# Kernel optimization log

Measured on AMD Instinct MI355X. Metric: run time of the kernel, lower is better.

The kernel has to match this reference:

```python
import jax, jax.numpy as jnp
import numpy as np

B, N, HID, HEADS, LAYERS, POOL = 2, 2048, 256, 4, 2, 128
D = HID // HEADS  # per-head dim


def attn_pool(x, w1, b1, w2, b2):
    # x: [B,N,HID]; mask is all-ones in this module's forward, so plain softmax
    s = jnp.tanh(x @ w1 + b1) @ w2 + b2            # [B,N]
    a = jax.nn.softmax(s, axis=-1)                  # [B,N]
    return jnp.einsum('bn,bnc->bc', a, x)           # [B,HID]


def gat_layer(x, adj_mask, proj_w, a_src, a_dst):
    # x: [B,N,HID] -> h: [B,N,HEADS,D]
    h = (x @ proj_w).reshape(x.shape[0], x.shape[1], HEADS, D)
    src = jnp.einsum('bnhd,hd->bnh', h, a_src)      # [B,N,H]
    dst = jnp.einsum('bnhd,hd->bnh', h, a_dst)      # [B,N,H]
    logits = src[:, :, None, :] + dst[:, None, :, :]  # [B,i,j,H]
    logits = jnp.where(logits >= 0, logits, 0.2 * logits)  # leaky_relu(0.2)
    logits = jnp.where(adj_mask[..., None], logits, jnp.float32(-1e9))
    attn = jax.nn.softmax(logits, axis=2)           # softmax over j (neighbors)
    out = jnp.einsum('bijh,bjhd->bihd', attn, h)
    return out.reshape(x.shape[0], x.shape[1], HEADS * D)


def setup_inputs() -> dict:
    key = jax.random.key(0)
    ks = jax.random.split(key, 16)
    sd = 0.05
    gene_expr = jax.random.normal(ks[0], (B, N), dtype=jnp.float32)
    gene_adj = jax.random.randint(ks[1], (B, N, N), 0, 2, dtype=jnp.int32)
    in_w = jax.random.normal(ks[2], (HID,), dtype=jnp.float32) * sd
    in_b = jax.random.normal(ks[3], (HID,), dtype=jnp.float32) * sd
    proj_w = jax.random.normal(ks[4], (LAYERS, HID, HID), dtype=jnp.float32) * sd
    attn_src = jax.random.normal(ks[5], (LAYERS, HEADS, D), dtype=jnp.float32) * sd
    attn_dst = jax.random.normal(ks[6], (LAYERS, HEADS, D), dtype=jnp.float32) * sd
    pool_w1 = jax.random.normal(ks[7], (LAYERS, HID, POOL), dtype=jnp.float32) * sd
    pool_b1 = jax.random.normal(ks[8], (LAYERS, POOL), dtype=jnp.float32) * sd
    pool_w2 = jax.random.normal(ks[9], (LAYERS, POOL), dtype=jnp.float32) * sd
    pool_b2 = jax.random.normal(ks[10], (LAYERS,), dtype=jnp.float32) * sd
    ip_w1 = jax.random.normal(ks[11], (HID, POOL), dtype=jnp.float32) * sd
    ip_b1 = jax.random.normal(ks[12], (POOL,), dtype=jnp.float32) * sd
    ip_w2 = jax.random.normal(ks[13], (POOL,), dtype=jnp.float32) * sd
    ip_b2 = jax.random.normal(ks[14], (), dtype=jnp.float32) * sd
    return dict(gene_expr=gene_expr, gene_adj=gene_adj, in_w=in_w, in_b=in_b,
                proj_w=proj_w, attn_src=attn_src, attn_dst=attn_dst,
                pool_w1=pool_w1, pool_b1=pool_b1, pool_w2=pool_w2, pool_b2=pool_b2,
                ip_w1=ip_w1, ip_b1=ip_b1, ip_w2=ip_w2, ip_b2=ip_b2)


def reference(gene_expr, gene_adj, in_w, in_b, proj_w, attn_src, attn_dst,
              pool_w1, pool_b1, pool_w2, pool_b2, ip_w1, ip_b1, ip_w2, ip_b2):
    # input_proj: Linear(1, HID) on gene_expr[...,None], then relu
    x = jax.nn.relu(gene_expr[:, :, None] * in_w + in_b)  # [B,N,HID]
    raw_pooled = attn_pool(x, ip_w1, ip_b1, ip_w2, ip_b2)
    adj_mask = gene_adj > 0
    node_outs, pooled_outs = [], []
    cur = x
    for l in range(LAYERS):
        cur = gat_layer(cur, adj_mask, proj_w[l], attn_src[l], attn_dst[l])
        cur = jax.nn.elu(cur)
        node_outs.append(cur)
        pooled_outs.append(attn_pool(cur, pool_w1[l], pool_b1[l], pool_w2[l], pool_b2[l]))
    # (raw_pooled, node_out_0, node_out_1, pooled_0, pooled_1); final_pooled == pooled_outs[-1]
    return (raw_pooled, *node_outs, *pooled_outs)
```

## Files before the change

kernel.cpp:

```cpp
#include <hip/hip_runtime.h>
#include <hip/hip_bf16.h>

#define B_ 2
#define N_ 2048
#define HID_ 256
#define HEADS_ 4
#define D_ 64
#define POOL_ 128
#define LOG2E_ 1.4426950408889634f

typedef __bf16 bf16;
typedef __bf16 bf16x8 __attribute__((ext_vector_type(8)));
typedef float f32x4 __attribute__((ext_vector_type(4)));

__device__ __forceinline__ float fast_tanh(float x) {
    x = fminf(fmaxf(x, -15.f), 15.f);
    float t = __expf(2.f * x);
    return (t - 1.f) / (t + 1.f);
}

__global__ void k_setup(const int* __restrict__ adj, unsigned* __restrict__ am,
                        const float* __restrict__ ge, const float* __restrict__ iw,
                        const float* __restrict__ ib, bf16* __restrict__ xb,
                        const float* __restrict__ proj_w, const float* __restrict__ ipw1,
                        const float* __restrict__ pw1, bf16* __restrict__ wT0,
                        bf16* __restrict__ wT1, bf16* __restrict__ ipw1T,
                        bf16* __restrict__ w1T0, bf16* __restrict__ w1T1) {
    int blk = blockIdx.x, tid = threadIdx.x;
    if (blk < 32768) {
        int gid = blk * 256 + tid;
        int v = adj[gid];
        unsigned long long mask = __ballot(v > 0);
        int lane = tid & 63;
        if (lane == 0) am[gid >> 5] = (unsigned)mask;
        else if (lane == 32) am[gid >> 5] = (unsigned)(mask >> 32);
    } else if (blk < 36864) {
        int row = blk - 32768;
        float g = ge[row];
        float v = fmaxf(g * iw[tid] + ib[tid], 0.f);
        xb[row * HID_ + tid] = (bf16)v;
    } else {
        int o = (blk - 36864) * 256 + tid;
        const float* src; bf16* dst; int Nc, loc;
        if (o < 65536)       { src = proj_w;         dst = wT0;   Nc = 256; loc = o; }
        else if (o < 131072) { src = proj_w + 65536; dst = wT1;   Nc = 256; loc = o - 65536; }
        else if (o < 163840) { src = ipw1;           dst = ipw1T; Nc = 128; loc = o - 131072; }
        else if (o < 196608) { src = pw1;            dst = w1T0;  Nc = 128; loc = o - 163840; }
        else                 { src = pw1 + 32768;    dst = w1T1;  Nc = 128; loc = o - 196608; }
        int n = loc >> 8, k = loc & 255;
        dst[loc] = (bf16)src[k * Nc + n];
    }
}

__device__ __forceinline__ void pool_sw_body(const bf16* __restrict__ A,
                                             const bf16* __restrict__ W1T,
                                             const float* __restrict__ b1,
                                             const float* __restrict__ w2,
                                             const float* __restrict__ b2,
                                             float* __restrict__ part,
                                             float* __restrict__ pz,
                                             int slot, int b, int ch, char* smemraw) {
    int n0 = ch * 16;
    int tid = threadIdx.x;
    int w = tid >> 6, lane = tid & 63, r = lane & 15, g = lane >> 4;
    const bf16* ap = A + ((long long)(b * N_ + n0) + r) * 256 + g * 8;
    f32x4 acc[2] = {{0,0,0,0},{0,0,0,0}};
    for (int ks = 0; ks < 256; ks += 32) {
        bf16x8 af = *(const bf16x8*)(ap + ks);
        #pragma unroll
        for (int nf = 0; nf < 2; ++nf) {
            bf16x8 bfr = *(const bf16x8*)(W1T + (w * 32 + nf * 16 + r) * 256 + ks + g * 8);
            acc[nf] = __builtin_amdgcn_mfma_f32_16x16x32_bf16(af, bfr, acc[nf], 0, 0, 0);
        }
    }
    float b1v[2], w2v[2];
    #pragma unroll
    for (int nf = 0; nf < 2; ++nf) {
        b1v[nf] = b1[w * 32 + nf * 16 + r];
        w2v[nf] = w2[w * 32 + nf * 16 + r];
    }
    float (*pred)[16] = (float (*)[16])smemraw;
    float* el = (float*)(smemraw + 256);
    #pragma unroll
    for (int q = 0; q < 4; ++q) {
        float p = fast_tanh(acc[0][q] + b1v[0]) * w2v[0] + fast_tanh(acc[1][q] + b1v[1]) * w2v[1];
        p += __shfl_xor(p, 1); p += __shfl_xor(p, 2);
        p += __shfl_xor(p, 4); p += __shfl_xor(p, 8);
        if (r == 0) pred[w][g * 4 + q] = p;
    }
    __syncthreads();
    if (tid < 16) {
        float s = pred[0][tid] + pred[1][tid] + pred[2][tid] + pred[3][tid] + b2[0];
        el[tid] = __expf(s);
    }
    __syncthreads();
    if (tid == 0) {
        float z = 0.f;
        #pragma unroll
        for (int n = 0; n < 16; ++n) z += el[n];
        pz[(slot * B_ + b) * 128 + ch] = z;
    }
    const bf16* xp = A + (long long)(b * N_ + n0) * 256 + tid;
    float accum = 0.f;
    #pragma unroll
    for (int n = 0; n < 16; ++n) accum += el[n] * (float)xp[n * 256];
    part[(((long long)slot * B_ + b) * 128 + ch) * 256 + tid] = accum;
}

__global__ __launch_bounds__(256) void k_gemm_h_pool(const bf16* __restrict__ A,
                                                     const bf16* __restrict__ WT,
                                                     const float* __restrict__ as,
                                                     const float* __restrict__ ad,
                                                     bf16* __restrict__ hbT,
                                                     float* __restrict__ srcM,
                                                     float* __restrict__ dstT,
                                                     const bf16* __restrict__ W1T,
                                                     const float* __restrict__ b1,
                                                     const float* __restrict__ w2,
                                                     const float* __restrict__ b2,
                                                     float* __restrict__ part,
                                                     float* __restrict__ pz, int slot) {
    __shared__ __align__(16) char smem[16640];
    int blk = blockIdx.x;
    if (blk >= 256) {
        int pb = blk - 256;
        pool_sw_body(A, W1T, b1, w2, b2, part, pz, slot, pb >> 7, pb & 127, smem);
        return;
    }
    int i0 = (blk & 63) * 64, hd = blk >> 6;
    int n0 = hd * 64;
    int w = threadIdx.x >> 6, lane = threadIdx.x & 63, r = lane & 15, g = lane >> 4;
    const bf16* ap = A + (i0 + w * 16 + r) * 256 + g * 8;
    f32x4 acc[4] = {{0,0,0,0},{0,0,0,0},{0,0,0,0},{0,0,0,0}};
    for (int ks = 0; ks < 256; ks += 32) {
        bf16x8 af = *(const bf16x8*)(ap + ks);
        #pragma unroll
        for (int nf = 0; nf < 4; ++nf) {
            bf16x8 bfr = *(const bf16x8*)(WT + (n0 + nf * 16 + r) * 256 + ks + g * 8);
            acc[nf] = __builtin_amdgcn_mfma_f32_16x16x32_bf16(af, bfr, acc[nf], 0, 0, 0);
        }
    }
    int b = i0 >> 11, nbase = i0 & 2047;
    int bh = b * HEADS_ + hd;
    float asv[4], adv[4];
    #pragma unroll
    for (int nf = 0; nf < 4; ++nf) {
        asv[nf] = as[hd * 64 + nf * 16 + r] * LOG2E_;
        adv[nf] = ad[hd * 64 + nf * 16 + r] * LOG2E_;
    }
    float (*tr)[65] = (float (*)[65])smem;
    #pragma unroll
    for (int q = 0; q < 4; ++q) {
        int ln = w * 16 + g * 4 + q;
        float ps = 0.f, pd = 0.f;
        #pragma unroll
        for (int nf = 0; nf < 4; ++nf) {
            float v = acc[nf][q];
            ps += v * asv[nf];
            pd += v * adv[nf];
            tr[nf * 16 + r][ln] = v;
        }
        ps += __shfl_xor(ps, 1); ps += __shfl_xor(ps, 2);
        ps += __shfl_xor(ps, 4); ps += __shfl_xor(ps, 8);
        pd += __shfl_xor(pd, 1); pd += __shfl_xor(pd, 2);
        pd += __shfl_xor(pd, 4); pd += __shfl_xor(pd, 8);
        if (r == 0) {
            srcM[bh * N_ + nbase + ln] = ps;
            dstT[bh * N_ + nbase + ln] = pd;
        }
    }
    __syncthreads();
    int ld = threadIdx.x >> 2, ln0 = (threadIdx.x & 3) * 16;
    bf16x8 o0, o1;
    #pragma unroll
    for (int e = 0; e < 8; ++e) {
        o0[e] = (bf16)tr[ld][ln0 + e];
        o1[e] = (bf16)tr[ld][ln0 + 8 + e];
    }
    bf16* hp = hbT + ((long long)bh * D_ + ld) * N_ + nbase + ln0;
    *(bf16x8*)(hp) = o0;
    *(bf16x8*)(hp + 8) = o1;
}

__global__ __launch_bounds__(256) void k_pool_sw(const bf16* __restrict__ A,
                                                 const bf16* __restrict__ W1T,
                                                 const float* __restrict__ b1,
                                                 const float* __restrict__ w2,
                                                 const float* __restrict__ b2,
                                                 float* __restrict__ part,
                                                 float* __restrict__ pz, int slot) {
    __shared__ __align__(16) char smem[320];
    pool_sw_body(A, W1T, b1, w2, b2, part, pz, slot, blockIdx.y, blockIdx.x, smem);
}

__global__ __launch_bounds__(1024, 8) void k_attn(const float* __restrict__ srcM,
                                                  const float* __restrict__ dstT,
                                                  const unsigned* __restrict__ am,
                                                  const bf16* __restrict__ hbT,
                                                  float* __restrict__ nodeOut,
                                                  bf16* __restrict__ xbNext) {
    int it = blockIdx.x, hd = blockIdx.y, b = blockIdx.z;
    int i0 = it * 32;
    int tid = threadIdx.x;
    int w = tid >> 6, lane = tid & 63, r = lane & 15, g = lane >> 4;
    int rg = w >> 3, wj = w & 7;
    int bh = b * HEADS_ + hd;
    const float* drow = dstT + bh * N_;
    const bf16* vbase = hbT + (long long)bh * D_ * N_;

    __shared__ __align__(16) char smem[34816];
    bf16* vt = (bf16*)smem;
    float (*accs)[16][68] = (float (*)[16][68])smem;
    __shared__ float lred[16][16];

    int i = i0 + rg * 16 + r;
    const unsigned* mrow = am + ((long long)(b * N_ + i)) * 64;
    unsigned mw[8];
    #pragma unroll
    for (int t = 0; t < 8; ++t) mw[t] = mrow[t * 8 + wj];
    float sv = srcM[bh * N_ + i];

    f32x4 acc[4] = {{0,0,0,0},{0,0,0,0},{0,0,0,0},{0,0,0,0}};
    float l = 0.f;

    bf16x8 st[2];
    #pragma unroll
    for (int k = 0; k < 2; ++k) {
        int s = tid + k * 1024, d = s >> 5, seg = s & 31;
        st[k] = *(const bf16x8*)(vbase + d * N_ + seg * 8);
    }

    #pragma unroll
    for (int t = 0; t < 8; ++t) {
        #pragma unroll
        for (int k = 0; k < 2; ++k) {
            int s = tid + k * 1024, d = s >> 5, seg = s & 31;
            *(bf16x8*)(vt + d * 264 + seg * 8) = st[k];
        }
        __syncthreads();
        if (t < 7) {
            #pragma unroll
            for (int k = 0; k < 2; ++k) {
                int s = tid + k * 1024, d = s >> 5, seg = s & 31;
                st[k] = *(const bf16x8*)(vbase + d * N_ + (t + 1) * 256 + seg * 8);
            }
        }
        int jb = t * 256 + wj * 32 + g * 8;
        float4 dv0 = *(const float4*)(drow + jb);
        float4 dv1 = *(const float4*)(drow + jb + 4);
        unsigned mb = (mw[t] >> (g * 8)) & 0xFFu;
        float dd[8] = {dv0.x, dv0.y, dv0.z, dv0.w, dv1.x, dv1.y, dv1.z, dv1.w};
        bf16x8 af;
        float es[8];
        #pragma unroll
        for (int tt = 0; tt < 8; ++tt) {
            float s2 = sv + dd[tt];
            float lv = fmaxf(s2, 0.2f * s2);
            float e2 = __builtin_amdgcn_exp2f(lv);
            e2 = ((mb >> tt) & 1u) ? e2 : 0.f;
            es[tt] = e2;
            af[tt] = (bf16)e2;
        }
        l += ((es[0] + es[1]) + (es[2] + es[3])) + ((es[4] + es[5]) + (es[6] + es[7]));
        #pragma unroll
        for (int nf = 0; nf < 4; ++nf) {
            bf16x8 vf = *(const bf16x8*)(vt + (nf * 16 + r) * 264 + wj * 32 + g * 8);
            acc[nf] = __builtin_amdgcn_mfma_f32_16x16x32_bf16(af, vf, acc[nf], 0, 0, 0);
        }
        __syncthreads();
    }

    l += __shfl_xor(l, 16);
    l += __shfl_xor(l, 32);
    if (g == 0) lred[w][r] = l;

    #pragma unroll
    for (int ph = 0; ph < 2; ++ph) {
        if (rg == ph) {
            #pragma unroll
            for (int nf = 0; nf < 4; ++nf)
                #pragma unroll
                for (int q = 0; q < 4; ++q)
                    accs[wj][g * 4 + q][nf * 16 + r] = acc[nf][q];
        }
        __syncthreads();
        {
            int rr = tid >> 6;
            int cc = tid & 63;
            float ls = 0.f, v = 0.f;
            #pragma unroll
            for (int w2 = 0; w2 < 8; ++w2) {
                ls += lred[ph * 8 + w2][rr];
                v += accs[w2][rr][cc];
            }
            v /= ls;
            float o = v > 0.f ? v : expm1f(v);
            int idx = (b * N_ + i0 + ph * 16 + rr) * HID_ + hd * D_ + cc;
            nodeOut[idx] = o;
            xbNext[idx] = (bf16)o;
        }
        __syncthreads();
    }
}

__global__ __launch_bounds__(256) void k_pool_finals(const float* __restrict__ part,
                                                     const float* __restrict__ pz,
                                                     float* __restrict__ outRaw,
                                                     float* __restrict__ pool0,
                                                     float* __restrict__ pool1) {
    int slot = blockIdx.x >> 1, b = blockIdx.x & 1;
    int tid = threadIdx.x;
    int lane = tid & 63, w = tid >> 6;
    float z = (tid < 128) ? pz[(slot * B_ + b) * 128 + tid] : 0.f;
    #pragma unroll
    for (int o = 1; o < 64; o <<= 1) z += __shfl_xor(z, o);
    __shared__ float red[4];
    if (lane == 0) red[w] = z;
    __syncthreads();
    float Z = red[0] + red[1] + red[2] + red[3];
    float acc = 0.f;
    #pragma unroll 8
    for (int ch = 0; ch < 128; ++ch)
        acc += part[(((long long)slot * B_ + b) * 128 + ch) * 256 + tid];
    float* out = slot == 0 ? outRaw : (slot == 1 ? pool0 : pool1);
    out[b * HID_ + tid] = acc / Z;
}

extern "C" void kernel_launch(void* const* d_in, const int* in_sizes, int n_in,
                              void* d_out, int out_size, void* d_ws, size_t ws_size,
                              hipStream_t stream) {
    const float* ge     = (const float*)d_in[0];
    const int*   adj    = (const int*)d_in[1];
    const float* in_w   = (const float*)d_in[2];
    const float* in_b   = (const float*)d_in[3];
    const float* proj_w = (const float*)d_in[4];
    const float* a_src  = (const float*)d_in[5];
    const float* a_dst  = (const float*)d_in[6];
    const float* pw1    = (const float*)d_in[7];
    const float* pb1    = (const float*)d_in[8];
    const float* pw2    = (const float*)d_in[9];
    const float* pb2    = (const float*)d_in[10];
    const float* ipw1   = (const float*)d_in[11];
    const float* ipb1   = (const float*)d_in[12];
    const float* ipw2   = (const float*)d_in[13];
    const float* ipb2   = (const float*)d_in[14];

    char* ws = (char*)d_ws;
    bf16*     xb    = (bf16*)(ws + 0);
    bf16*     hbT   = (bf16*)(ws + 2097152);
    float*    srcM  = (float*)(ws + 4194304);
    float*    dstT  = (float*)(ws + 4259840);
    unsigned* am    = (unsigned*)(ws + 4325376);
    bf16*     wT0   = (bf16*)(ws + 5373952);
    bf16*     wT1   = wT0 + 65536;
    bf16*     ipw1T = wT1 + 65536;
    bf16*     w1T0  = ipw1T + 32768;
    bf16*     w1T1  = w1T0 + 32768;
    float*    part  = (float*)(ws + 5832704);
    float*    pz    = (float*)(ws + 6619136);

    float* outRaw = (float*)d_out;
    float* node0  = outRaw + 512;
    float* node1  = node0 + 1048576;
    float* pool0  = node1 + 1048576;
    float* pool1  = pool0 + 512;

    k_setup<<<37760, 256, 0, stream>>>(adj, am, ge, in_w, in_b, xb,
                                       proj_w, ipw1, pw1, wT0, wT1, ipw1T, w1T0, w1T1);

    k_gemm_h_pool<<<512, 256, 0, stream>>>(xb, wT0, a_src, a_dst, hbT, srcM, dstT,
                                           ipw1T, ipb1, ipw2, ipb2, part, pz, 0);
    k_attn<<<dim3(64, 4, 2), 1024, 0, stream>>>(srcM, dstT, am, hbT, node0, xb);

    k_gemm_h_pool<<<512, 256, 0, stream>>>(xb, wT1, a_src + 256, a_dst + 256, hbT, srcM, dstT,
                                           w1T0, pb1, pw2, pb2, part, pz, 1);
    k_attn<<<dim3(64, 4, 2), 1024, 0, stream>>>(srcM, dstT, am, hbT, node1, xb);

    k_pool_sw<<<dim3(128, B_), 256, 0, stream>>>(xb, w1T1, pb1 + POOL_, pw2 + 1, pb2 + 1,
                                                 part, pz, 2);
    k_pool_finals<<<6, 256, 0, stream>>>(part, pz, outRaw, pool0, pool1);
}
```

Measured before the change: 104.8 us.

## Factor leaky-relu exponent into precomputed per-node exp2 products

```diff
diff --git a/kernel.cpp b/kernel.cpp
--- a/kernel.cpp
+++ b/kernel.cpp
@@ -112,8 +112,8 @@
                                                      const float* __restrict__ as,
                                                      const float* __restrict__ ad,
                                                      bf16* __restrict__ hbT,
-                                                     float* __restrict__ srcM,
-                                                     float* __restrict__ dstT,
+                                                     float2* __restrict__ srcEE,
+                                                     float2* __restrict__ dstFF,
                                                      const bf16* __restrict__ W1T,
                                                      const float* __restrict__ b1,
                                                      const float* __restrict__ w2,
@@ -165,8 +165,10 @@
         pd += __shfl_xor(pd, 1); pd += __shfl_xor(pd, 2);
         pd += __shfl_xor(pd, 4); pd += __shfl_xor(pd, 8);
         if (r == 0) {
-            srcM[bh * N_ + nbase + ln] = ps;
-            dstT[bh * N_ + nbase + ln] = pd;
+            srcEE[bh * N_ + nbase + ln] =
+                make_float2(__builtin_amdgcn_exp2f(ps), __builtin_amdgcn_exp2f(0.2f * ps));
+            dstFF[bh * N_ + nbase + ln] =
+                make_float2(__builtin_amdgcn_exp2f(pd), __builtin_amdgcn_exp2f(0.2f * pd));
         }
     }
     __syncthreads();
@@ -193,8 +195,8 @@
     pool_sw_body(A, W1T, b1, w2, b2, part, pz, slot, blockIdx.y, blockIdx.x, smem);
 }
 
-__global__ __launch_bounds__(1024, 8) void k_attn(const float* __restrict__ srcM,
-                                                  const float* __restrict__ dstT,
+__global__ __launch_bounds__(1024, 8) void k_attn(const float2* __restrict__ srcEE,
+                                                  const float2* __restrict__ dstFF,
                                                   const unsigned* __restrict__ am,
                                                   const bf16* __restrict__ hbT,
                                                   float* __restrict__ nodeOut,
@@ -205,7 +207,7 @@
     int w = tid >> 6, lane = tid & 63, r = lane & 15, g = lane >> 4;
     int rg = w >> 3, wj = w & 7;
     int bh = b * HEADS_ + hd;
-    const float* drow = dstT + bh * N_;
+    const float2* ffrow = dstFF + bh * N_;
     const bf16* vbase = hbT + (long long)bh * D_ * N_;
 
     __shared__ __align__(16) char smem[34816];
@@ -218,7 +220,9 @@
     unsigned mw[8];
     #pragma unroll
     for (int t = 0; t < 8; ++t) mw[t] = mrow[t * 8 + wj];
-    float sv = srcM[bh * N_ + i];
+    float2 ee = srcEE[bh * N_ + i];
+    float E = ee.x, Ep = ee.y;
+    float T = __builtin_amdgcn_rcpf(Ep);
 
     f32x4 acc[4] = {{0,0,0,0},{0,0,0,0},{0,0,0,0},{0,0,0,0}};
     float l = 0.f;
@@ -246,17 +250,19 @@
             }
         }
         int jb = t * 256 + wj * 32 + g * 8;
-        float4 dv0 = *(const float4*)(drow + jb);
-        float4 dv1 = *(const float4*)(drow + jb + 4);
+        float4 q0 = *(const float4*)(ffrow + jb);
+        float4 q1 = *(const float4*)(ffrow + jb + 2);
+        float4 q2 = *(const float4*)(ffrow + jb + 4);
+        float4 q3 = *(const float4*)(ffrow + jb + 6);
+        float Fv[8]  = {q0.x, q0.z, q1.x, q1.z, q2.x, q2.z, q3.x, q3.z};
+        float Fpv[8] = {q0.y, q0.w, q1.y, q1.w, q2.y, q2.w, q3.y, q3.w};
         unsigned mb = (mw[t] >> (g * 8)) & 0xFFu;
-        float dd[8] = {dv0.x, dv0.y, dv0.z, dv0.w, dv1.x, dv1.y, dv1.z, dv1.w};
         bf16x8 af;
         float es[8];
         #pragma unroll
         for (int tt = 0; tt < 8; ++tt) {
-            float s2 = sv + dd[tt];
-            float lv = fmaxf(s2, 0.2f * s2);
-            float e2 = __builtin_amdgcn_exp2f(lv);
+            bool c = Fpv[tt] >= T;
+            float e2 = (c ? E : Ep) * (c ? Fv[tt] : Fpv[tt]);
             e2 = ((mb >> tt) & 1u) ? e2 : 0.f;
             es[tt] = e2;
             af[tt] = (bf16)e2;
@@ -348,16 +354,16 @@
     char* ws = (char*)d_ws;
     bf16*     xb    = (bf16*)(ws + 0);
     bf16*     hbT   = (bf16*)(ws + 2097152);
-    float*    srcM  = (float*)(ws + 4194304);
-    float*    dstT  = (float*)(ws + 4259840);
-    unsigned* am    = (unsigned*)(ws + 4325376);
-    bf16*     wT0   = (bf16*)(ws + 5373952);
+    float2*   srcEE = (float2*)(ws + 4194304);
+    float2*   dstFF = (float2*)(ws + 4325376);
+    unsigned* am    = (unsigned*)(ws + 4456448);
+    bf16*     wT0   = (bf16*)(ws + 5505024);
     bf16*     wT1   = wT0 + 65536;
     bf16*     ipw1T = wT1 + 65536;
     bf16*     w1T0  = ipw1T + 32768;
     bf16*     w1T1  = w1T0 + 32768;
-    float*    part  = (float*)(ws + 5832704);
-    float*    pz    = (float*)(ws + 6619136);
+    float*    part  = (float*)(ws + 5963776);
+    float*    pz    = (float*)(ws + 6750208);
 
     float* outRaw = (float*)d_out;
     float* node0  = outRaw + 512;
@@ -368,13 +374,13 @@
     k_setup<<<37760, 256, 0, stream>>>(adj, am, ge, in_w, in_b, xb,
                                        proj_w, ipw1, pw1, wT0, wT1, ipw1T, w1T0, w1T1);
 
-    k_gemm_h_pool<<<512, 256, 0, stream>>>(xb, wT0, a_src, a_dst, hbT, srcM, dstT,
+    k_gemm_h_pool<<<512, 256, 0, stream>>>(xb, wT0, a_src, a_dst, hbT, srcEE, dstFF,
                                            ipw1T, ipb1, ipw2, ipb2, part, pz, 0);
-    k_attn<<<dim3(64, 4, 2), 1024, 0, stream>>>(srcM, dstT, am, hbT, node0, xb);
-
-    k_gemm_h_pool<<<512, 256, 0, stream>>>(xb, wT1, a_src + 256, a_dst + 256, hbT, srcM, dstT,
+    k_attn<<<dim3(64, 4, 2), 1024, 0, stream>>>(srcEE, dstFF, am, hbT, node0, xb);
+
+    k_gemm_h_pool<<<512, 256, 0, stream>>>(xb, wT1, a_src + 256, a_dst + 256, hbT, srcEE, dstFF,
                                            w1T0, pb1, pw2, pb2, part, pz, 1);
-    k_attn<<<dim3(64, 4, 2), 1024, 0, stream>>>(srcM, dstT, am, hbT, node1, xb);
+    k_attn<<<dim3(64, 4, 2), 1024, 0, stream>>>(srcEE, dstFF, am, hbT, node1, xb);
 
     k_pool_sw<<<dim3(128, B_), 256, 0, stream>>>(xb, w1T1, pb1 + POOL_, pw2 + 1, pb2 + 1,
                                                  part, pz, 2);
```

New measurement: 110.4 us. 1.05x slower.

## Double rows per attention block and compute row sums via MFMA

Applied to the files above, without the earlier changes.

```diff
diff --git a/kernel.cpp b/kernel.cpp
--- a/kernel.cpp
+++ b/kernel.cpp
@@ -193,17 +193,17 @@
     pool_sw_body(A, W1T, b1, w2, b2, part, pz, slot, blockIdx.y, blockIdx.x, smem);
 }
 
-__global__ __launch_bounds__(1024, 8) void k_attn(const float* __restrict__ srcM,
+__global__ __launch_bounds__(1024, 4) void k_attn(const float* __restrict__ srcM,
                                                   const float* __restrict__ dstT,
                                                   const unsigned* __restrict__ am,
                                                   const bf16* __restrict__ hbT,
                                                   float* __restrict__ nodeOut,
                                                   bf16* __restrict__ xbNext) {
     int it = blockIdx.x, hd = blockIdx.y, b = blockIdx.z;
-    int i0 = it * 32;
+    int i0 = it * 64;
     int tid = threadIdx.x;
     int w = tid >> 6, lane = tid & 63, r = lane & 15, g = lane >> 4;
-    int rg = w >> 3, wj = w & 7;
+    int rg = w >> 2, wj = w & 3;
     int bh = b * HEADS_ + hd;
     const float* drow = dstT + bh * N_;
     const bf16* vbase = hbT + (long long)bh * D_ * N_;
@@ -211,17 +211,22 @@
     __shared__ __align__(16) char smem[34816];
     bf16* vt = (bf16*)smem;
     float (*accs)[16][68] = (float (*)[16][68])smem;
-    __shared__ float lred[16][16];
 
     int i = i0 + rg * 16 + r;
     const unsigned* mrow = am + ((long long)(b * N_ + i)) * 64;
-    unsigned mw[8];
-    #pragma unroll
-    for (int t = 0; t < 8; ++t) mw[t] = mrow[t * 8 + wj];
+    unsigned mw[8][2];
+    #pragma unroll
+    for (int t = 0; t < 8; ++t) {
+        mw[t][0] = mrow[t * 8 + wj * 2];
+        mw[t][1] = mrow[t * 8 + wj * 2 + 1];
+    }
     float sv = srcM[bh * N_ + i];
 
     f32x4 acc[4] = {{0,0,0,0},{0,0,0,0},{0,0,0,0},{0,0,0,0}};
-    float l = 0.f;
+    f32x4 accl = {0,0,0,0};
+    bf16x8 ones;
+    #pragma unroll
+    for (int e = 0; e < 8; ++e) ones[e] = (bf16)1.0f;
 
     bf16x8 st[2];
     #pragma unroll
@@ -245,43 +250,46 @@
                 st[k] = *(const bf16x8*)(vbase + d * N_ + (t + 1) * 256 + seg * 8);
             }
         }
-        int jb = t * 256 + wj * 32 + g * 8;
-        float4 dv0 = *(const float4*)(drow + jb);
-        float4 dv1 = *(const float4*)(drow + jb + 4);
-        unsigned mb = (mw[t] >> (g * 8)) & 0xFFu;
-        float dd[8] = {dv0.x, dv0.y, dv0.z, dv0.w, dv1.x, dv1.y, dv1.z, dv1.w};
-        bf16x8 af;
-        float es[8];
-        #pragma unroll
-        for (int tt = 0; tt < 8; ++tt) {
-            float s2 = sv + dd[tt];
-            float lv = fmaxf(s2, 0.2f * s2);
-            float e2 = __builtin_amdgcn_exp2f(lv);
-            e2 = ((mb >> tt) & 1u) ? e2 : 0.f;
-            es[tt] = e2;
-            af[tt] = (bf16)e2;
-        }
-        l += ((es[0] + es[1]) + (es[2] + es[3])) + ((es[4] + es[5]) + (es[6] + es[7]));
-        #pragma unroll
-        for (int nf = 0; nf < 4; ++nf) {
-            bf16x8 vf = *(const bf16x8*)(vt + (nf * 16 + r) * 264 + wj * 32 + g * 8);
-            acc[nf] = __builtin_amdgcn_mfma_f32_16x16x32_bf16(af, vf, acc[nf], 0, 0, 0);
+        #pragma unroll
+        for (int oct = 0; oct < 2; ++oct) {
+            int jb = wj * 64 + oct * 32 + g * 8;
+            int jg = t * 256 + jb;
+            float4 dv0 = *(const float4*)(drow + jg);
+            float4 dv1 = *(const float4*)(drow + jg + 4);
+            unsigned mb = (mw[t][oct] >> (g * 8)) & 0xFFu;
+            float dd[8] = {dv0.x, dv0.y, dv0.z, dv0.w, dv1.x, dv1.y, dv1.z, dv1.w};
+            bf16x8 af;
+            #pragma unroll
+            for (int tt = 0; tt < 8; ++tt) {
+                float s2 = sv + dd[tt];
+                float lv = fmaxf(s2, 0.2f * s2);
+                float e2 = __builtin_amdgcn_exp2f(lv);
+                e2 = ((mb >> tt) & 1u) ? e2 : 0.f;
+                af[tt] = (bf16)e2;
+            }
+            #pragma unroll
+            for (int nf = 0; nf < 4; ++nf) {
+                bf16x8 vf = *(const bf16x8*)(vt + (nf * 16 + r) * 264 + jb);
+                acc[nf] = __builtin_amdgcn_mfma_f32_16x16x32_bf16(af, vf, acc[nf], 0, 0, 0);
+            }
+            accl = __builtin_amdgcn_mfma_f32_16x16x32_bf16(af, ones, accl, 0, 0, 0);
         }
         __syncthreads();
     }
 
-    l += __shfl_xor(l, 16);
-    l += __shfl_xor(l, 32);
-    if (g == 0) lred[w][r] = l;
-
-    #pragma unroll
-    for (int ph = 0; ph < 2; ++ph) {
+    #pragma unroll
+    for (int ph = 0; ph < 4; ++ph) {
         if (rg == ph) {
             #pragma unroll
             for (int nf = 0; nf < 4; ++nf)
                 #pragma unroll
                 for (int q = 0; q < 4; ++q)
                     accs[wj][g * 4 + q][nf * 16 + r] = acc[nf][q];
+            if (r == 0) {
+                #pragma unroll
+                for (int q = 0; q < 4; ++q)
+                    accs[wj][g * 4 + q][64] = accl[q];
+            }
         }
         __syncthreads();
         {
@@ -289,12 +297,12 @@
             int cc = tid & 63;
             float ls = 0.f, v = 0.f;
             #pragma unroll
-            for (int w2 = 0; w2 < 8; ++w2) {
-                ls += lred[ph * 8 + w2][rr];
+            for (int w2 = 0; w2 < 4; ++w2) {
+                ls += accs[w2][rr][64];
                 v += accs[w2][rr][cc];
             }
             v /= ls;
-            float o = v > 0.f ? v : expm1f(v);
+            float o = v > 0.f ? v : (__builtin_amdgcn_exp2f(v * LOG2E_) - 1.f);
             int idx = (b * N_ + i0 + ph * 16 + rr) * HID_ + hd * D_ + cc;
             nodeOut[idx] = o;
             xbNext[idx] = (bf16)o;
@@ -370,11 +378,11 @@
 
     k_gemm_h_pool<<<512, 256, 0, stream>>>(xb, wT0, a_src, a_dst, hbT, srcM, dstT,
                                            ipw1T, ipb1, ipw2, ipb2, part, pz, 0);
-    k_attn<<<dim3(64, 4, 2), 1024, 0, stream>>>(srcM, dstT, am, hbT, node0, xb);
+    k_attn<<<dim3(32, 4, 2), 1024, 0, stream>>>(srcM, dstT, am, hbT, node0, xb);
 
     k_gemm_h_pool<<<512, 256, 0, stream>>>(xb, wT1, a_src + 256, a_dst + 256, hbT, srcM, dstT,
                                            w1T0, pb1, pw2, pb2, part, pz, 1);
-    k_attn<<<dim3(64, 4, 2), 1024, 0, stream>>>(srcM, dstT, am, hbT, node1, xb);
+    k_attn<<<dim3(32, 4, 2), 1024, 0, stream>>>(srcM, dstT, am, hbT, node1, xb);
 
     k_pool_sw<<<dim3(128, B_), 256, 0, stream>>>(xb, w1T1, pb1 + POOL_, pw2 + 1, pb2 + 1,
                                                  part, pz, 2);
```

Result: faster. 100.5 us (-4.1%).
